# Optimization experiments

Hardware: AMD Instinct MI355X
Metric: run time of the kernel (lower is better)

The kernel has to match this reference:

```python
import jax, jax.numpy as jnp
import numpy as np

NH = 16      # num_heads
D = 128      # head_dim
C = 64       # chunk_size
EPS = 1e-12  # F.normalize eps


def setup_inputs() -> dict:
    key = jax.random.key(0)
    ks = jax.random.split(key, 12)
    B, L, H = 4, 4096, 2048
    std = 0.02
    f32 = jnp.float32
    inp = {
        "hidden_states": jax.random.normal(ks[0], (B, L, H), f32),
        # torch nn.Linear weights are [out_features, in_features]
        "q_w": jax.random.normal(ks[1], (NH * D, H), f32) * std,
        "q_b": jnp.zeros((NH * D,), f32),
        "k_w": jax.random.normal(ks[2], (NH * D, H), f32) * std,
        "k_b": jnp.zeros((NH * D,), f32),
        "v_w": jax.random.normal(ks[3], (NH * D, H), f32) * std,
        "v_b": jnp.zeros((NH * D,), f32),
        "a_w": jax.random.normal(ks[4], (NH, H), f32) * std,
        "a_b": jnp.zeros((NH,), f32),
        "b_w": jax.random.normal(ks[5], (NH, H), f32) * std,
        "b_b": jnp.zeros((NH,), f32),
        "og_w": jax.random.normal(ks[6], (NH * D, H), f32) * std,  # no bias
        "o_w": jax.random.normal(ks[7], (H, NH * D), f32) * std,
        "o_b": jnp.zeros((H,), f32),
    }
    return inp


def _l2norm(x):
    n = jnp.linalg.norm(x, axis=-1, keepdims=True)
    return x / jnp.maximum(n, EPS)


def reference(hidden_states, q_w, q_b, k_w, k_b, v_w, v_b,
              a_w, a_b, b_w, b_b, og_w, o_w, o_b):
    B, L, H = hidden_states.shape
    nh, d, c = NH, D, C
    hs = hidden_states

    q = (hs @ q_w.T + q_b).reshape(B, L, nh, d)
    k = (hs @ k_w.T + k_b).reshape(B, L, nh, d)
    v = (hs @ v_w.T + v_b).reshape(B, L, nh, d)
    # alpha = sigmoid(hs @ a_w.T + a_b) is computed in the original module but
    # never affects the output (alpha_mean / log_alpha are dead code) -> omitted.
    beta = jax.nn.softplus(hs @ b_w.T + b_b)            # [B,L,nh]

    scale = float(d) ** 0.5
    qn = _l2norm(q / scale)                              # normalize makes /scale moot, kept faithful
    kn = _l2norm(k / scale)
    gv = beta[..., None] * v                             # [B,L,nh,d]

    nchunks = L // c

    def to_chunks(x):  # [B,L,nh,d] -> [B,nchunks,nh,c,d]
        return x.reshape(B, nchunks, c, nh, d).transpose(0, 1, 3, 2, 4)

    qc, kc, gvc = to_chunks(qn), to_chunks(kn), to_chunks(gv)

    attn = jnp.einsum('bnhid,bnhjd->bnhij', qc, kc)      # per-chunk QK^T
    pos = jnp.arange(c, dtype=jnp.float32)
    dist = jnp.clip(pos[None, :] - pos[:, None], 0.0, None)   # (j-i) clamped >=0
    decay = jnp.exp(-0.1 * dist)
    causal = pos[None, :] <= pos[:, None]                # keep j<=i, zero j>i
    mask = jnp.where(causal, decay, 0.0)                 # [c,c]
    out = jnp.einsum('bnhij,bnhjd->bnhid', attn * mask, gvc)

    out = out.transpose(0, 1, 3, 2, 4).reshape(B, L, nh * d)
    gate = jax.nn.silu(hs @ og_w.T)                      # output_gate has no bias
    out = out * gate
    return out @ o_w.T + o_b
```

## Files before the change

kernel.cpp:

```cpp
#include <hip/hip_runtime.h>


typedef __bf16 bf16x8 __attribute__((ext_vector_type(8)));
typedef float f32x4 __attribute__((ext_vector_type(4)));

typedef __attribute__((address_space(1))) const unsigned int g_u32;
typedef __attribute__((address_space(3))) unsigned int l_u32;

__device__ __forceinline__ void cp16(const unsigned short* g, unsigned short* l) {
  __builtin_amdgcn_global_load_lds((g_u32*)g, (l_u32*)l, 16, 0, 0);
}

__device__ __forceinline__ unsigned short f2bf(float x) {
  unsigned u = __builtin_bit_cast(unsigned, x);
  u += 0x7fffu + ((u >> 16) & 1u);
  return (unsigned short)(u >> 16);
}
__device__ __forceinline__ float bf2f(unsigned short h) {
  return __builtin_bit_cast(float, (unsigned)h << 16);
}
__device__ __forceinline__ unsigned pk2(float a, float b) {
  return (unsigned)f2bf(a) | ((unsigned)f2bf(b) << 16);
}

__global__ __launch_bounds__(256) void cvt_bf16(const float* __restrict__ in,
                                                unsigned short* __restrict__ out,
                                                int n) {
  int i = (blockIdx.x * 256 + threadIdx.x) * 8;
  if (i >= n) return;
  float4 f0 = *(const float4*)(in + i);
  float4 f1 = *(const float4*)(in + i + 4);
  uint4 u;
  u.x = pk2(f0.x, f0.y); u.y = pk2(f0.z, f0.w);
  u.z = pk2(f1.x, f1.y); u.w = pk2(f1.z, f1.w);
  *(uint4*)(out + i) = u;
}

__global__ __launch_bounds__(256) void build_bias(
    const float* __restrict__ qb, const float* __restrict__ kb,
    const float* __restrict__ vb, float* __restrict__ bias_cat) {
  int i = blockIdx.x * 256 + threadIdx.x;
  float v = 0.f;
  if (i < 2048) v = qb[i];
  else if (i < 4096) v = kb[i - 2048];
  else if (i < 6144) v = vb[i - 4096];
  bias_cat[i] = v;
}

__global__ __launch_bounds__(256) void beta_kernel(
    const float* __restrict__ hs, const float* __restrict__ bw,
    const float* __restrict__ bb, float* __restrict__ beta,
    unsigned short* __restrict__ hsb) {
  __shared__ float row[2048];
  __shared__ float part[16][17];
  const int m = blockIdx.x;
  const float* src = hs + (size_t)m * 2048;
  for (int i = threadIdx.x; i < 512; i += 256)
    ((float4*)row)[i] = ((const float4*)src)[i];
  __syncthreads();
  if (hsb) {
    int e = threadIdx.x * 8;
    uint4 u;
    u.x = pk2(row[e], row[e + 1]);     u.y = pk2(row[e + 2], row[e + 3]);
    u.z = pk2(row[e + 4], row[e + 5]); u.w = pk2(row[e + 6], row[e + 7]);
    *(uint4*)(hsb + (size_t)m * 2048 + e) = u;
  }
  const int h = threadIdx.x >> 4, j = threadIdx.x & 15;
  const float* w = bw + h * 2048;
  float s = 0.f;
  #pragma unroll 8
  for (int kk = 0; kk < 128; kk++) {
    int k = j + (kk << 4);
    s += row[k] * w[k];
  }
  part[h][j] = s;
  __syncthreads();
  if (threadIdx.x < 16) {
    int hh = threadIdx.x;
    float t = bb[hh];
    #pragma unroll
    for (int j2 = 0; j2 < 16; j2++) t += part[hh][j2];
    beta[(size_t)m * 16 + hh] = fmaxf(t, 0.f) + log1pf(__expf(-fabsf(t)));
  }
}

template <int EPI, int N, int K>
__global__ __launch_bounds__(256, 4) void gemm_async(
    const unsigned short* __restrict__ A, const unsigned short* __restrict__ Bw,
    const float* __restrict__ bias, const float* __restrict__ beta,
    void* __restrict__ Cv) {
  __shared__ __align__(16) unsigned short As[128 * 32];
  __shared__ __align__(16) unsigned short Bs[128 * 32];
  const int tid = threadIdx.x;
  const int m0 = blockIdx.y * 128;
  const int n0 = blockIdx.x * 128;
  const int wid = tid >> 6, lane = tid & 63;
  const int wm = wid >> 1, wn = wid & 1;
  const int quad = lane >> 4, l16 = lane & 15;

  const int srow = tid >> 2;
  const int scol = ((tid & 3) ^ ((tid >> 3) & 3)) << 3;
  const unsigned short* Ag0 = A + (size_t)(m0 + srow) * K + scol;
  const unsigned short* Ag1 = Ag0 + (size_t)64 * K;
  const unsigned short* Bg0 = Bw + (size_t)(n0 + srow) * K + scol;
  const unsigned short* Bg1 = Bg0 + (size_t)64 * K;
  unsigned short* la0 = &As[tid * 8];
  unsigned short* la1 = &As[(tid + 256) * 8];
  unsigned short* lb0 = &Bs[tid * 8];
  unsigned short* lb1 = &Bs[(tid + 256) * 8];

  const int pchunk = (quad ^ ((l16 >> 1) & 3)) << 3;

  f32x4 acc[4][4] = {};

  for (int kb = 0; kb < K; kb += 32) {
    cp16(Ag0 + kb, la0);
    cp16(Ag1 + kb, la1);
    cp16(Bg0 + kb, lb0);
    cp16(Bg1 + kb, lb1);
    __syncthreads();
    bf16x8 af[4], bfr[4];
    #pragma unroll
    for (int mi = 0; mi < 4; mi++)
      af[mi] = *(const bf16x8*)&As[(wm * 64 + mi * 16 + l16) * 32 + pchunk];
    #pragma unroll
    for (int ni = 0; ni < 4; ni++)
      bfr[ni] = *(const bf16x8*)&Bs[(wn * 64 + ni * 16 + l16) * 32 + pchunk];
    #pragma unroll
    for (int mi = 0; mi < 4; mi++)
      #pragma unroll
      for (int ni = 0; ni < 4; ni++)
        acc[mi][ni] = __builtin_amdgcn_mfma_f32_16x16x32_bf16(
            af[mi], bfr[ni], acc[mi][ni], 0, 0, 0);
    __syncthreads();
  }

  if (EPI == 0) {
    const int mode = n0 >> 11;
    unsigned short* outp =
        (unsigned short*)Cv + (size_t)mode * ((size_t)16384 * 2048);
    const int head = (n0 >> 7) & 15;
    #pragma unroll
    for (int mi = 0; mi < 4; mi++) {
      #pragma unroll
      for (int r = 0; r < 4; r++) {
        const int row = m0 + wm * 64 + mi * 16 + quad * 4 + r;
        const float bsc = (mode == 2) ? beta[(size_t)row * 16 + head] : 1.f;
        #pragma unroll
        for (int ni = 0; ni < 4; ni++) {
          const int col = n0 + wn * 64 + ni * 16 + l16;
          float x = acc[mi][ni][r] + bias[col];
          if (mode == 2) x *= bsc;
          if (mode == 3) x = x / (1.f + __expf(-x));
          outp[(size_t)row * 2048 + (col & 2047)] = f2bf(x);
        }
      }
    }
  } else {
    #pragma unroll
    for (int mi = 0; mi < 4; mi++)
      #pragma unroll
      for (int r = 0; r < 4; r++) {
        const int row = m0 + wm * 64 + mi * 16 + quad * 4 + r;
        #pragma unroll
        for (int ni = 0; ni < 4; ni++) {
          const int col = n0 + wn * 64 + ni * 16 + l16;
          ((float*)Cv)[(size_t)row * N + col] = acc[mi][ni][r] + bias[col];
        }
      }
  }
}

constexpr int GLDW = 40;
template <int EPI, bool ABF16>
__global__ __launch_bounds__(256) void gemm_bt(
    const void* __restrict__ Av, const float* __restrict__ Bw,
    const float* __restrict__ bias, const float* __restrict__ beta,
    void* __restrict__ Cv, int M, int N, int K) {
  __shared__ unsigned short As[128 * GLDW];
  __shared__ unsigned short Bs[128 * GLDW];
  const int tid = threadIdx.x;
  const int m0 = blockIdx.y * 128;
  const int n0 = blockIdx.x * 128;
  const int wid = tid >> 6, lane = tid & 63;
  const int wm = wid >> 1, wn = wid & 1;
  const int quad = lane >> 4, l16 = lane & 15;
  const int srow = tid >> 1, skh = (tid & 1) << 4;

  f32x4 acc[4][4] = {};
  const float* Bg = Bw + (size_t)(n0 + srow) * K + skh;

  for (int kb = 0; kb < K; kb += 32) {
    if (ABF16) {
      const unsigned short* Ag =
          (const unsigned short*)Av + (size_t)(m0 + srow) * K + kb + skh;
      uint4 u0 = ((const uint4*)Ag)[0];
      uint4 u1 = ((const uint4*)Ag)[1];
      uint4* d = (uint4*)&As[srow * GLDW + skh];
      d[0] = u0; d[1] = u1;
    } else {
      const float* Ag = (const float*)Av + (size_t)(m0 + srow) * K + kb + skh;
      float4 f0 = ((const float4*)Ag)[0];
      float4 f1 = ((const float4*)Ag)[1];
      float4 f2 = ((const float4*)Ag)[2];
      float4 f3 = ((const float4*)Ag)[3];
      unsigned* d = (unsigned*)&As[srow * GLDW + skh];
      d[0] = pk2(f0.x, f0.y); d[1] = pk2(f0.z, f0.w);
      d[2] = pk2(f1.x, f1.y); d[3] = pk2(f1.z, f1.w);
      d[4] = pk2(f2.x, f2.y); d[5] = pk2(f2.z, f2.w);
      d[6] = pk2(f3.x, f3.y); d[7] = pk2(f3.z, f3.w);
    }
    {
      const float* Bgk = Bg + kb;
      float4 f0 = ((const float4*)Bgk)[0];
      float4 f1 = ((const float4*)Bgk)[1];
      float4 f2 = ((const float4*)Bgk)[2];
      float4 f3 = ((const float4*)Bgk)[3];
      unsigned* d = (unsigned*)&Bs[srow * GLDW + skh];
      d[0] = pk2(f0.x, f0.y); d[1] = pk2(f0.z, f0.w);
      d[2] = pk2(f1.x, f1.y); d[3] = pk2(f1.z, f1.w);
      d[4] = pk2(f2.x, f2.y); d[5] = pk2(f2.z, f2.w);
      d[6] = pk2(f3.x, f3.y); d[7] = pk2(f3.z, f3.w);
    }
    __syncthreads();
    bf16x8 af[4], bfr[4];
    #pragma unroll
    for (int mi = 0; mi < 4; mi++)
      af[mi] = *(const bf16x8*)&As[(wm * 64 + mi * 16 + l16) * GLDW + (quad << 3)];
    #pragma unroll
    for (int ni = 0; ni < 4; ni++)
      bfr[ni] = *(const bf16x8*)&Bs[(wn * 64 + ni * 16 + l16) * GLDW + (quad << 3)];
    #pragma unroll
    for (int mi = 0; mi < 4; mi++)
      #pragma unroll
      for (int ni = 0; ni < 4; ni++)
        acc[mi][ni] = __builtin_amdgcn_mfma_f32_16x16x32_bf16(
            af[mi], bfr[ni], acc[mi][ni], 0, 0, 0);
    __syncthreads();
  }

  #pragma unroll
  for (int mi = 0; mi < 4; mi++) {
    #pragma unroll
    for (int r = 0; r < 4; r++) {
      const int row = m0 + wm * 64 + mi * 16 + quad * 4 + r;
      float bsc = 1.f;
      if (EPI == 1) bsc = beta[(size_t)row * 16 + blockIdx.x];
      #pragma unroll
      for (int ni = 0; ni < 4; ni++) {
        const int col = n0 + wn * 64 + ni * 16 + l16;
        float x = acc[mi][ni][r];
        if (EPI != 2) x += bias[col];
        if (EPI == 1) x *= bsc;
        if (EPI == 2) x = x / (1.f + __expf(-x));
        if (EPI == 3)
          ((float*)Cv)[(size_t)row * N + col] = x;
        else
          ((unsigned short*)Cv)[(size_t)row * N + col] = f2bf(x);
      }
    }
  }
}

constexpr int QK_LDW = 132;
constexpr int GT_LDW = 66;
constexpr int SS_LDW = 68;

__global__ __launch_bounds__(256) void attn_kernel(
    const unsigned short* __restrict__ qn, const unsigned short* __restrict__ kn,
    const unsigned short* __restrict__ gvp, const unsigned short* __restrict__ gate,
    unsigned short* __restrict__ y) {
  __shared__ unsigned short qs[64 * QK_LDW];
  __shared__ unsigned short ks[64 * QK_LDW];
  __shared__ unsigned short gst[128 * GT_LDW];
  __shared__ unsigned short Ss[64 * SS_LDW];

  const int tid = threadIdx.x;
  const int m0 = blockIdx.x * 64;
  const int h = blockIdx.y;
  const size_t gbase = (size_t)m0 * 2048 + (size_t)h * 128;

  #pragma unroll
  for (int it = 0; it < 4; it++) {
    int e = tid + it * 256;
    int i = e >> 4;
    int c = (e & 15) << 3;
    size_t g = gbase + (size_t)i * 2048 + c;
    *(uint4*)&qs[i * QK_LDW + c] = *(const uint4*)&qn[g];
    *(uint4*)&ks[i * QK_LDW + c] = *(const uint4*)&kn[g];
    uint4 gvv = *(const uint4*)&gvp[g];
    unsigned short tmp[8];
    *(uint4*)tmp = gvv;
    #pragma unroll
    for (int t = 0; t < 8; t++) gst[(c + t) * GT_LDW + i] = tmp[t];
  }
  __syncthreads();

  {
    const int rr = tid >> 2;
    const int seg = (tid & 3) * 32;
    float ssq = 0.f, ssk = 0.f;
    #pragma unroll
    for (int k2 = 0; k2 < 32; k2 += 2) {
      unsigned uq = *(const unsigned*)&qs[rr * QK_LDW + seg + k2];
      unsigned uk = *(const unsigned*)&ks[rr * QK_LDW + seg + k2];
      float a = bf2f((unsigned short)(uq & 0xffff)), b = bf2f((unsigned short)(uq >> 16));
      float c2 = bf2f((unsigned short)(uk & 0xffff)), d2 = bf2f((unsigned short)(uk >> 16));
      ssq += a * a + b * b;
      ssk += c2 * c2 + d2 * d2;
    }
    ssq += __shfl_xor(ssq, 1); ssq += __shfl_xor(ssq, 2);
    ssk += __shfl_xor(ssk, 1); ssk += __shfl_xor(ssk, 2);
    float iq = rsqrtf(fmaxf(ssq, 1e-24f));
    float ik = rsqrtf(fmaxf(ssk, 1e-24f));
    #pragma unroll
    for (int k2 = 0; k2 < 32; k2 += 2) {
      unsigned uq = *(const unsigned*)&qs[rr * QK_LDW + seg + k2];
      unsigned uk = *(const unsigned*)&ks[rr * QK_LDW + seg + k2];
      float a = bf2f((unsigned short)(uq & 0xffff)), b = bf2f((unsigned short)(uq >> 16));
      float c2 = bf2f((unsigned short)(uk & 0xffff)), d2 = bf2f((unsigned short)(uk >> 16));
      *(unsigned*)&qs[rr * QK_LDW + seg + k2] = pk2(a * iq, b * iq);
      *(unsigned*)&ks[rr * QK_LDW + seg + k2] = pk2(c2 * ik, d2 * ik);
    }
  }
  __syncthreads();

  const int w = tid >> 6;
  const int lane = tid & 63;
  const int quad = lane >> 4, l16 = lane & 15;

  {
    f32x4 acc[4] = {};
    #pragma unroll
    for (int kst = 0; kst < 4; kst++) {
      bf16x8 a = *(const bf16x8*)&qs[(w * 16 + l16) * QK_LDW + kst * 32 + (quad << 3)];
      #pragma unroll
      for (int ni = 0; ni < 4; ni++) {
        bf16x8 b = *(const bf16x8*)&ks[(ni * 16 + l16) * QK_LDW + kst * 32 + (quad << 3)];
        acc[ni] = __builtin_amdgcn_mfma_f32_16x16x32_bf16(a, b, acc[ni], 0, 0, 0);
      }
    }
    #pragma unroll
    for (int ni = 0; ni < 4; ni++)
      #pragma unroll
      for (int r = 0; r < 4; r++) {
        int row = w * 16 + quad * 4 + r;
        int col = ni * 16 + l16;
        float val = (col <= row) ? acc[ni][r] : 0.f;
        Ss[row * SS_LDW + col] = f2bf(val);
      }
  }
  __syncthreads();

  {
    f32x4 acc[8] = {};
    #pragma unroll
    for (int kst = 0; kst < 2; kst++) {
      bf16x8 a = *(const bf16x8*)&Ss[(w * 16 + l16) * SS_LDW + kst * 32 + (quad << 3)];
      #pragma unroll
      for (int nd = 0; nd < 8; nd++) {
        bf16x8 b = *(const bf16x8*)&gst[(nd * 16 + l16) * GT_LDW + kst * 32 + (quad << 3)];
        acc[nd] = __builtin_amdgcn_mfma_f32_16x16x32_bf16(a, b, acc[nd], 0, 0, 0);
      }
    }
    #pragma unroll
    for (int nd = 0; nd < 8; nd++)
      #pragma unroll
      for (int r = 0; r < 4; r++) {
        int row = w * 16 + quad * 4 + r;
        int col = nd * 16 + l16;
        size_t g = gbase + (size_t)row * 2048 + col;
        float gt = bf2f(gate[g]);
        y[g] = f2bf(acc[nd][r] * gt);
      }
  }
}

extern "C" void kernel_launch(void* const* d_in, const int* in_sizes, int n_in,
                              void* d_out, int out_size, void* d_ws, size_t ws_size,
                              hipStream_t stream) {
  const float* hs   = (const float*)d_in[0];
  const float* q_w  = (const float*)d_in[1];
  const float* q_b  = (const float*)d_in[2];
  const float* k_w  = (const float*)d_in[3];
  const float* k_b  = (const float*)d_in[4];
  const float* v_w  = (const float*)d_in[5];
  const float* v_b  = (const float*)d_in[6];
  const float* b_w  = (const float*)d_in[9];
  const float* b_b  = (const float*)d_in[10];
  const float* og_w = (const float*)d_in[11];
  const float* o_w  = (const float*)d_in[12];
  const float* o_b  = (const float*)d_in[13];

  const int M = 16384, K = 2048;
  const size_t MB64 = 67108864;

  const size_t OFF_HSB  = 4 * MB64;
  const size_t OFF_WCAT = OFF_HSB + MB64;
  const size_t OFF_OWB  = OFF_WCAT + 33554432;
  const size_t OFF_BETA = OFF_OWB + 8388608;
  const size_t OFF_BIAS = OFF_BETA + 1048576;
  const size_t NEED     = OFF_BIAS + 32768;

  char* ws = (char*)d_ws;

  if (ws_size >= NEED) {
    unsigned short* qy   = (unsigned short*)ws;
    unsigned short* knb  = (unsigned short*)(ws + MB64);
    unsigned short* gv   = (unsigned short*)(ws + 2 * MB64);
    unsigned short* gate = (unsigned short*)(ws + 3 * MB64);
    unsigned short* hsb  = (unsigned short*)(ws + OFF_HSB);
    unsigned short* wcat = (unsigned short*)(ws + OFF_WCAT);
    unsigned short* owb  = (unsigned short*)(ws + OFF_OWB);
    float*          beta = (float*)(ws + OFF_BETA);
    float*          bias = (float*)(ws + OFF_BIAS);

    const int NW = 4194304;
    cvt_bf16<<<NW / 2048, 256, 0, stream>>>(q_w,  wcat,          NW);
    cvt_bf16<<<NW / 2048, 256, 0, stream>>>(k_w,  wcat + NW,     NW);
    cvt_bf16<<<NW / 2048, 256, 0, stream>>>(v_w,  wcat + 2 * NW, NW);
    cvt_bf16<<<NW / 2048, 256, 0, stream>>>(og_w, wcat + 3 * NW, NW);
    cvt_bf16<<<NW / 2048, 256, 0, stream>>>(o_w,  owb,           NW);
    build_bias<<<32, 256, 0, stream>>>(q_b, k_b, v_b, bias);
    beta_kernel<<<M, 256, 0, stream>>>(hs, b_w, b_b, beta, hsb);

    gemm_async<0, 8192, 2048><<<dim3(64, 128), 256, 0, stream>>>(
        hsb, wcat, bias, beta, qy);

    attn_kernel<<<dim3(256, 16), 256, 0, stream>>>(qy, knb, gv, gate, qy);

    gemm_async<3, 2048, 2048><<<dim3(16, 128), 256, 0, stream>>>(
        qy, owb, o_b, nullptr, (float*)d_out);
  } else {
    unsigned short* qy   = (unsigned short*)ws;
    unsigned short* knb  = (unsigned short*)(ws + MB64);
    unsigned short* gv   = (unsigned short*)(ws + 2 * MB64);
    unsigned short* gate = (unsigned short*)(ws + 3 * MB64);
    float*          beta = (float*)(ws + 4 * MB64);

    beta_kernel<<<M, 256, 0, stream>>>(hs, b_w, b_b, beta, nullptr);
    dim3 gg(16, 128);
    gemm_bt<0, false><<<gg, 256, 0, stream>>>(hs, q_w, q_b, nullptr, qy, M, 2048, K);
    gemm_bt<0, false><<<gg, 256, 0, stream>>>(hs, k_w, k_b, nullptr, knb, M, 2048, K);
    gemm_bt<1, false><<<gg, 256, 0, stream>>>(hs, v_w, v_b, beta, gv, M, 2048, K);
    gemm_bt<2, false><<<gg, 256, 0, stream>>>(hs, og_w, nullptr, nullptr, gate, M, 2048, K);
    attn_kernel<<<dim3(256, 16), 256, 0, stream>>>(qy, knb, gv, gate, qy);
    gemm_bt<3, true><<<gg, 256, 0, stream>>>(qy, o_w, o_b, nullptr, (float*)d_out, M, 2048, K);
  }
}
```

Baseline: 1.223 ms.

## Replace 128x128 GEMM with 256x256 tile, 4-stage async LDS pipeline

The bf16 MFMA GEMM grows from 128x128 tiles with 256 threads and a single LDS buffer to 256x256 tiles with 512 threads. A 4-deep ring of global_load_lds buffers prefetches three k-steps ahead, and waits use s_waitcnt vmcnt plus a single barrier per iteration in place of two __syncthreads. It also raises wave priority around MFMA bursts, changes the LDS swizzle, and writes outputs with nontemporal stores. The goal is to hide global load latency and raise arithmetic intensity, at the cost of 128KB of LDS, more accumulator registers, lower occupancy, and fewer blocks for the smaller output GEMM.

```diff
diff --git a/kernel.cpp b/kernel.cpp
--- a/kernel.cpp
+++ b/kernel.cpp
@@ -85,66 +85,99 @@
 }
 
 template <int EPI, int N, int K>
-__global__ __launch_bounds__(256, 4) void gemm_async(
+__global__ __launch_bounds__(512, 2) void gemm256(
     const unsigned short* __restrict__ A, const unsigned short* __restrict__ Bw,
     const float* __restrict__ bias, const float* __restrict__ beta,
     void* __restrict__ Cv) {
-  __shared__ __align__(16) unsigned short As[128 * 32];
-  __shared__ __align__(16) unsigned short Bs[128 * 32];
+  constexpr int NT = K / 32;
+  __shared__ __align__(16) unsigned short As[4 * 8192];
+  __shared__ __align__(16) unsigned short Bs[4 * 8192];
   const int tid = threadIdx.x;
-  const int m0 = blockIdx.y * 128;
-  const int n0 = blockIdx.x * 128;
+  const int m0 = blockIdx.y * 256;
+  const int n0 = blockIdx.x * 256;
   const int wid = tid >> 6, lane = tid & 63;
-  const int wm = wid >> 1, wn = wid & 1;
+  const int wm = wid >> 2, wn = wid & 3;
   const int quad = lane >> 4, l16 = lane & 15;
 
-  const int srow = tid >> 2;
-  const int scol = ((tid & 3) ^ ((tid >> 3) & 3)) << 3;
-  const unsigned short* Ag0 = A + (size_t)(m0 + srow) * K + scol;
-  const unsigned short* Ag1 = Ag0 + (size_t)64 * K;
-  const unsigned short* Bg0 = Bw + (size_t)(n0 + srow) * K + scol;
-  const unsigned short* Bg1 = Bg0 + (size_t)64 * K;
-  unsigned short* la0 = &As[tid * 8];
-  unsigned short* la1 = &As[(tid + 256) * 8];
-  unsigned short* lb0 = &Bs[tid * 8];
-  unsigned short* lb1 = &Bs[(tid + 256) * 8];
-
-  const int pchunk = (quad ^ ((l16 >> 1) & 3)) << 3;
-
-  f32x4 acc[4][4] = {};
-
-  for (int kb = 0; kb < K; kb += 32) {
-    cp16(Ag0 + kb, la0);
-    cp16(Ag1 + kb, la1);
-    cp16(Bg0 + kb, lb0);
-    cp16(Bg1 + kb, lb1);
-    __syncthreads();
+  const int trow = tid >> 2;
+  const int tch = ((tid & 3) ^ (trow & 3)) << 3;
+  const unsigned short* Ag = A + (size_t)(m0 + trow) * K + tch;
+  const unsigned short* Bg = Bw + (size_t)(n0 + trow) * K + tch;
+
+  const int chs = (quad ^ (l16 & 3)) << 4;
+  const int a_lane = (wm * 128 + l16) * 64 + chs;
+  const int b_lane = (wn * 64 + l16) * 64 + chs;
+
+  f32x4 acc[8][4] = {};
+
+  #pragma unroll
+  for (int tt = 0; tt < 3; ++tt) {
+    const size_t kk = (size_t)tt * 32;
+    unsigned short* la = As + tt * 8192 + tid * 8;
+    unsigned short* lb = Bs + tt * 8192 + tid * 8;
+    cp16(Ag + kk, la);
+    cp16(Ag + (size_t)128 * K + kk, la + 4096);
+    cp16(Bg + kk, lb);
+    cp16(Bg + (size_t)128 * K + kk, lb + 4096);
+  }
+  asm volatile("s_waitcnt vmcnt(8)" ::: "memory");
+  __builtin_amdgcn_s_barrier();
+
+  for (int t = 0; t < NT; ++t) {
+    const int cur = t & 3;
+    const int nb = (t + 3) & 3;
+    const size_t k3 = (size_t)((t + 3 < NT) ? (t + 3) : (NT - 1)) * 32;
+    const char* At = (const char*)As + cur * 16384 + a_lane;
+    const char* Bt = (const char*)Bs + cur * 16384 + b_lane;
+    unsigned short* la = As + nb * 8192 + tid * 8;
+    unsigned short* lb = Bs + nb * 8192 + tid * 8;
+
+    cp16(Ag + k3, la);
+    cp16(Ag + (size_t)128 * K + k3, la + 4096);
     bf16x8 af[4], bfr[4];
     #pragma unroll
-    for (int mi = 0; mi < 4; mi++)
-      af[mi] = *(const bf16x8*)&As[(wm * 64 + mi * 16 + l16) * 32 + pchunk];
-    #pragma unroll
-    for (int ni = 0; ni < 4; ni++)
-      bfr[ni] = *(const bf16x8*)&Bs[(wn * 64 + ni * 16 + l16) * 32 + pchunk];
+    for (int mi = 0; mi < 4; mi++) af[mi] = *(const bf16x8*)(At + mi * 1024);
+    #pragma unroll
+    for (int ni = 0; ni < 4; ni++) bfr[ni] = *(const bf16x8*)(Bt + ni * 1024);
+    __builtin_amdgcn_s_setprio(1);
     #pragma unroll
     for (int mi = 0; mi < 4; mi++)
       #pragma unroll
       for (int ni = 0; ni < 4; ni++)
         acc[mi][ni] = __builtin_amdgcn_mfma_f32_16x16x32_bf16(
             af[mi], bfr[ni], acc[mi][ni], 0, 0, 0);
-    __syncthreads();
-  }
+    __builtin_amdgcn_s_setprio(0);
+
+    cp16(Bg + k3, lb);
+    cp16(Bg + (size_t)128 * K + k3, lb + 4096);
+    #pragma unroll
+    for (int mi = 0; mi < 4; mi++) af[mi] = *(const bf16x8*)(At + (4 + mi) * 1024);
+    __builtin_amdgcn_s_setprio(1);
+    #pragma unroll
+    for (int mi = 0; mi < 4; mi++)
+      #pragma unroll
+      for (int ni = 0; ni < 4; ni++)
+        acc[4 + mi][ni] = __builtin_amdgcn_mfma_f32_16x16x32_bf16(
+            af[mi], bfr[ni], acc[4 + mi][ni], 0, 0, 0);
+    __builtin_amdgcn_s_setprio(0);
+
+    if (t != NT - 1) {
+      asm volatile("s_waitcnt vmcnt(8)" ::: "memory");
+      __builtin_amdgcn_s_barrier();
+    }
+  }
+  asm volatile("s_waitcnt vmcnt(0)" ::: "memory");
 
   if (EPI == 0) {
     const int mode = n0 >> 11;
     unsigned short* outp =
         (unsigned short*)Cv + (size_t)mode * ((size_t)16384 * 2048);
-    const int head = (n0 >> 7) & 15;
-    #pragma unroll
-    for (int mi = 0; mi < 4; mi++) {
+    const int head = ((n0 + wn * 64) >> 7) & 15;
+    #pragma unroll
+    for (int mi = 0; mi < 8; mi++) {
       #pragma unroll
       for (int r = 0; r < 4; r++) {
-        const int row = m0 + wm * 64 + mi * 16 + quad * 4 + r;
+        const int row = m0 + wm * 128 + mi * 16 + quad * 4 + r;
         const float bsc = (mode == 2) ? beta[(size_t)row * 16 + head] : 1.f;
         #pragma unroll
         for (int ni = 0; ni < 4; ni++) {
@@ -152,20 +185,23 @@
           float x = acc[mi][ni][r] + bias[col];
           if (mode == 2) x *= bsc;
           if (mode == 3) x = x / (1.f + __expf(-x));
-          outp[(size_t)row * 2048 + (col & 2047)] = f2bf(x);
+          __builtin_nontemporal_store(
+              f2bf(x), &outp[(size_t)row * 2048 + (col & 2047)]);
         }
       }
     }
   } else {
     #pragma unroll
-    for (int mi = 0; mi < 4; mi++)
+    for (int mi = 0; mi < 8; mi++)
       #pragma unroll
       for (int r = 0; r < 4; r++) {
-        const int row = m0 + wm * 64 + mi * 16 + quad * 4 + r;
+        const int row = m0 + wm * 128 + mi * 16 + quad * 4 + r;
         #pragma unroll
         for (int ni = 0; ni < 4; ni++) {
           const int col = n0 + wn * 64 + ni * 16 + l16;
-          ((float*)Cv)[(size_t)row * N + col] = acc[mi][ni][r] + bias[col];
+          __builtin_nontemporal_store(
+              acc[mi][ni][r] + bias[col],
+              &((float*)Cv)[(size_t)row * N + col]);
         }
       }
   }
@@ -424,12 +460,12 @@
     build_bias<<<32, 256, 0, stream>>>(q_b, k_b, v_b, bias);
     beta_kernel<<<M, 256, 0, stream>>>(hs, b_w, b_b, beta, hsb);
 
-    gemm_async<0, 8192, 2048><<<dim3(64, 128), 256, 0, stream>>>(
+    gemm256<0, 8192, 2048><<<dim3(32, 64), 512, 0, stream>>>(
         hsb, wcat, bias, beta, qy);
 
     attn_kernel<<<dim3(256, 16), 256, 0, stream>>>(qy, knb, gv, gate, qy);
 
-    gemm_async<3, 2048, 2048><<<dim3(16, 128), 256, 0, stream>>>(
+    gemm256<3, 2048, 2048><<<dim3(8, 64), 512, 0, stream>>>(
         qy, owb, o_b, nullptr, (float*)d_out);
   } else {
     unsigned short* qy   = (unsigned short*)ws;
```

New measurement: 1.251 ms. 1.02x slower.
